# Kernel optimization log

Measured on AMD Instinct MI355X. Metric: run time of the kernel, lower is better.

The kernel has to match this reference:

```python
import jax, jax.numpy as jnp
import numpy as np

B, N, D, H = 2, 2048, 1024, 16
DH = D // H            # 64
PH = 3 * DH            # 192 per-head proj dim (module quirk: 3*Dh per head)
P = H * PH             # 3072 total projection width


def setup_inputs() -> dict:
    key = jax.random.key(0)
    ks = jax.random.split(key, 8)
    s = 0.02
    return {
        "input": jax.random.normal(ks[0], (B, N, D), dtype=jnp.float32),
        "q_w": jax.random.normal(ks[1], (D, P), dtype=jnp.float32) * s,
        "q_b": jnp.zeros((P,), dtype=jnp.float32),
        "k_w": jax.random.normal(ks[2], (D, P), dtype=jnp.float32) * s,
        "k_b": jnp.zeros((P,), dtype=jnp.float32),
        "v_w": jax.random.normal(ks[3], (D, P), dtype=jnp.float32) * s,
        "v_b": jnp.zeros((P,), dtype=jnp.float32),
        "o_w": jax.random.normal(ks[4], (P, D), dtype=jnp.float32) * s,
        "o_b": jnp.zeros((D,), dtype=jnp.float32),
    }


def reference(input, q_w, q_b, k_w, k_b, v_w, v_b, o_w, o_b):
    def heads(y):  # [B,N,H*PH] -> [B,H,N,PH]
        return y.reshape(B, N, H, PH).transpose(0, 2, 1, 3)

    q_mat = heads(input @ q_w + q_b)
    # faithful to source: v_mat uses the 'k' projection, k_mat uses the 'v' projection
    v_mat = heads(input @ k_w + k_b)
    k_mat = heads(input @ v_w + v_b)

    scale = 1.0 / jnp.sqrt(jnp.float32(DH * H))  # sqrt(dim), per source
    scores = jnp.einsum('bhnd,bhmd->bhnm', q_mat, k_mat) * scale
    weights = jax.nn.softmax(scores, axis=-1)
    inter = jnp.einsum('bhnm,bhmd->bhnd', weights, v_mat)
    inter = inter.transpose(0, 2, 1, 3).reshape(B, N, P)  # b n (h d)
    return inter @ o_w + o_b
```

## Files before the change

kernel.cpp:

```cpp
#include <hip/hip_runtime.h>
#include <cstdint>
#include <cstddef>

typedef __bf16 bf16;
typedef __attribute__((ext_vector_type(8))) __bf16 bf16x8;
typedef __attribute__((ext_vector_type(4))) __bf16 bf16x4;
typedef __attribute__((ext_vector_type(2))) __bf16 bf16x2;
typedef __attribute__((ext_vector_type(4))) float f32x4;

#define MFMA_16x16x32(a, b, c) __builtin_amdgcn_mfma_f32_16x16x32_bf16((a), (b), (c), 0, 0, 0)

__device__ __forceinline__ void gload_lds16(const void* g, void* l) {
  __builtin_amdgcn_global_load_lds((__attribute__((address_space(1))) void*)g,
                                   (__attribute__((address_space(3))) void*)l,
                                   16, 0, 0);
}

__global__ __launch_bounds__(256) void cvt_x_kernel(const float* __restrict__ in,
                                                    bf16* __restrict__ out) {
  int i = blockIdx.x * 256 + threadIdx.x;
  float4 v = ((const float4*)in)[i];
  bf16x4 o = {(bf16)v.x, (bf16)v.y, (bf16)v.z, (bf16)v.w};
  ((bf16x4*)out)[i] = o;
}

__global__ __launch_bounds__(256) void transpose_cvt_kernel(const float* __restrict__ in,
                                                            bf16* __restrict__ out,
                                                            int R, int C) {
  __shared__ float tile[32][33];
  int tiles_c = C >> 5;
  int br = (int)blockIdx.x / tiles_c, bc = (int)blockIdx.x % tiles_c;
  int r0 = br << 5, c0 = bc << 5;
  int tr = threadIdx.x >> 5, tc = threadIdx.x & 31;
#pragma unroll
  for (int i = 0; i < 4; i++)
    tile[tr + 8 * i][tc] = in[(size_t)(r0 + tr + 8 * i) * C + c0 + tc];
  __syncthreads();
#pragma unroll
  for (int i = 0; i < 4; i++) {
    int oc = tr + 8 * i;
    out[(size_t)(c0 + oc) * R + r0 + tc] = (bf16)tile[tc][oc];
  }
}

__global__ __launch_bounds__(256) void transpose_cvt3_kernel(const float* __restrict__ q_w,
                                                             const float* __restrict__ v_w,
                                                             const float* __restrict__ k_w,
                                                             bf16* __restrict__ out) {
  __shared__ float tile[32][33];
  int widx = (int)blockIdx.x / 3072;
  int blk = (int)blockIdx.x % 3072;
  const float* in = widx == 0 ? q_w : (widx == 1 ? v_w : k_w);
  bf16* o = out + (size_t)widx * 3072 * 1024;
  int br = blk / 96, bc = blk % 96;
  int r0 = br << 5, c0 = bc << 5;
  int tr = threadIdx.x >> 5, tc = threadIdx.x & 31;
#pragma unroll
  for (int i = 0; i < 4; i++)
    tile[tr + 8 * i][tc] = in[(size_t)(r0 + tr + 8 * i) * 3072 + c0 + tc];
  __syncthreads();
#pragma unroll
  for (int i = 0; i < 4; i++) {
    int oc = tr + 8 * i;
    o[(size_t)(c0 + oc) * 1024 + r0 + tc] = (bf16)tile[tc][oc];
  }
}

__global__ __launch_bounds__(512, 2) void gemm_fused_qkv(
    const bf16* __restrict__ A, const bf16* __restrict__ Bt,
    const float* __restrict__ q_b, const float* __restrict__ v_b,
    const float* __restrict__ k_b,
    bf16* __restrict__ Qm, bf16* __restrict__ Km, bf16* __restrict__ Vt) {
  constexpr int K = 1024, NT = 16;
  __shared__ __align__(16) bf16 sA[2][2][128 * 32];
  __shared__ __align__(16) bf16 sB[2][192 * 64];

  int bid = blockIdx.x;
  int xcd = bid & 7, j = bid >> 3;
  int bm = xcd * 4 + (j & 3), bn = j >> 2;
  int m0 = bm << 7, n0 = bn * 192;

  int tid = threadIdx.x, lane = tid & 63, w = tid >> 6;
  int wr = w >> 2, wc = w & 3;
  int l15 = lane & 15, lg = lane >> 4;

  int sra = lane >> 2, sca = lane & 3;
  const bf16* gA = A + (size_t)(m0 + w * 16 + sra) * K + ((sca ^ ((sra >> 1) & 3)) * 8);
  int srb = lane >> 3, scb = lane & 7;
  const bf16* gB = Bt + (size_t)(n0 + w * 24 + srb) * K + ((scb ^ srb) * 8);

#define STAGE_AB(BUF, T)                                                   \
  {                                                                        \
    _Pragma("unroll") for (int kh = 0; kh < 2; kh++)                       \
        gload_lds16(gA + (size_t)(T) * 64 + kh * 32, &sA[BUF][kh][w * 512]); \
    _Pragma("unroll") for (int ii = 0; ii < 3; ii++)                       \
        gload_lds16(gB + (size_t)(ii * 8) * K + (T) * 64,                  \
                    &sB[BUF][(w * 3 + ii) * 512]);                         \
  }
#define VMCNT(N) asm volatile("s_waitcnt vmcnt(" #N ")" ::: "memory")
#define LGK0                                           \
  {                                                    \
    asm volatile("s_waitcnt lgkmcnt(0)" ::: "memory"); \
    __builtin_amdgcn_sched_barrier(0);                 \
  }

  int slotA = lg ^ ((l15 >> 1) & 3);
  int aBase = wr * 2048 + l15 * 32 + slotA * 8;
  int bBase = (wc * 48 + l15) * 64;
  int sB0 = (lg ^ (l15 & 7)) * 8;
  int sB1 = ((4 + lg) ^ (l15 & 7)) * 8;

#define RD_A(BUF, KH)                                                      \
  _Pragma("unroll") for (int mf = 0; mf < 4; mf++)                         \
      a[mf] = *(const bf16x8*)&sA[BUF][KH][aBase + mf * 512];
#define RD_B(BUF, SLOT)                                                    \
  _Pragma("unroll") for (int nf = 0; nf < 3; nf++)                         \
      b[nf] = *(const bf16x8*)&sB[BUF][bBase + nf * 1024 + (SLOT)];
#define MFMA12                                                             \
  _Pragma("unroll") for (int mf = 0; mf < 4; mf++)                         \
      _Pragma("unroll") for (int nf = 0; nf < 3; nf++)                     \
          acc[mf][nf] = MFMA_16x16x32(a[mf], b[nf], acc[mf][nf]);

  f32x4 acc[4][3];
#pragma unroll
  for (int mf = 0; mf < 4; mf++)
#pragma unroll
    for (int nf = 0; nf < 3; nf++) acc[mf][nf] = (f32x4){0.f, 0.f, 0.f, 0.f};

  STAGE_AB(0, 0);

#pragma unroll 2
  for (int s = 0; s < NT; s++) {
    int buf = s & 1, nbuf = buf ^ 1;
    int nxt = (s + 1) & (NT - 1);
    bf16x8 a[4], b[3];

    STAGE_AB(nbuf, nxt);
    VMCNT(5);
    __builtin_amdgcn_s_barrier();

    RD_A(buf, 0);
    RD_B(buf, sB0);
    LGK0;
    __builtin_amdgcn_s_setprio(1);
    MFMA12;
    __builtin_amdgcn_s_setprio(0);

    RD_A(buf, 1);
    RD_B(buf, sB1);
    LGK0;
    __builtin_amdgcn_s_barrier();
    __builtin_amdgcn_s_setprio(1);
    MFMA12;
    __builtin_amdgcn_s_setprio(0);
  }

  int seg = bn >> 4;
  int segbn = bn & 15;
  const float* bias = seg == 0 ? q_b : (seg == 1 ? v_b : k_b);
  bf16* outQK = seg == 0 ? Qm : Km;
#pragma unroll
  for (int mf = 0; mf < 4; mf++) {
#pragma unroll
    for (int nf = 0; nf < 3; nf++) {
      int colL = segbn * 192 + wc * 48 + nf * 16 + l15;
      int row0 = m0 + wr * 64 + mf * 16 + lg * 4;
      float bv = bias[colL];
      if (seg < 2) {
#pragma unroll
        for (int r = 0; r < 4; r++)
          outQK[(size_t)(row0 + r) * 3072 + colL] = (bf16)(acc[mf][nf][r] + bv);
      } else {
        int hh = colL / 192, dd = colL % 192;
        int bi = row0 >> 11, nn = row0 & 2047;
        bf16x4 pk = {(bf16)(acc[mf][nf][0] + bv), (bf16)(acc[mf][nf][1] + bv),
                     (bf16)(acc[mf][nf][2] + bv), (bf16)(acc[mf][nf][3] + bv)};
        *(bf16x4*)(Vt + (((size_t)bi * 16 + hh) * 192 + dd) * 2048 + nn) = pk;
      }
    }
  }
#undef STAGE_AB
#undef RD_A
#undef RD_B
#undef MFMA12
}

__global__ __launch_bounds__(256, 3) void gemm_oproj(const bf16* __restrict__ A,
                                                     const bf16* __restrict__ Bt,
                                                     const float* __restrict__ bias,
                                                     float* __restrict__ out) {
  constexpr int K = 3072, NT = 48;
  __shared__ __align__(16) bf16 sA[2][2][128 * 32];
  __shared__ __align__(16) bf16 sB[2][2][64 * 32];

  int bid = blockIdx.x;
  int xcd = bid & 7, j = bid >> 3;
  int bm = xcd * 4 + (j & 3), bn = j >> 2;
  int m0 = bm << 7, n0 = bn << 6;

  int tid = threadIdx.x, lane = tid & 63, w = tid >> 6;
  int wr = w >> 1, wc = w & 1;
  int l15 = lane & 15, lg = lane >> 4;

  int sra = lane >> 2, sca = lane & 3;
  int swzS = (sca ^ ((sra >> 1) & 3)) * 8;
  const bf16* gA = A + (size_t)(m0 + w * 32 + sra) * K + swzS;
  const bf16* gB = Bt + (size_t)(n0 + w * 16 + sra) * K + swzS;

#define O_STAGE(BUF, T)                                                     \
  {                                                                         \
    _Pragma("unroll") for (int kh = 0; kh < 2; kh++) {                      \
      _Pragma("unroll") for (int ii = 0; ii < 2; ii++)                      \
          gload_lds16(gA + (size_t)(ii * 16) * K + (T) * 64 + kh * 32,      \
                      &sA[BUF][kh][(w * 32 + ii * 16) * 32]);               \
      gload_lds16(gB + (size_t)(T) * 64 + kh * 32, &sB[BUF][kh][w * 512]);  \
    }                                                                       \
  }

  int slotA = lg ^ ((l15 >> 1) & 3);
  int aBase = (wr * 64 + l15) * 32 + slotA * 8;
  int bBase = (wc * 32 + l15) * 32 + slotA * 8;

#define O_RD(BUF, KH)                                                      \
  {                                                                        \
    _Pragma("unroll") for (int mf = 0; mf < 4; mf++)                       \
        a[mf] = *(const bf16x8*)&sA[BUF][KH][aBase + mf * 512];             \
    _Pragma("unroll") for (int nf = 0; nf < 2; nf++)                       \
        b[nf] = *(const bf16x8*)&sB[BUF][KH][bBase + nf * 512];             \
  }
#define O_MFMA8                                                            \
  _Pragma("unroll") for (int mf = 0; mf < 4; mf++)                         \
      _Pragma("unroll") for (int nf = 0; nf < 2; nf++)                     \
          acc[mf][nf] = MFMA_16x16x32(a[mf], b[nf], acc[mf][nf]);

  f32x4 acc[4][2];
#pragma unroll
  for (int mf = 0; mf < 4; mf++)
#pragma unroll
    for (int nf = 0; nf < 2; nf++) acc[mf][nf] = (f32x4){0.f, 0.f, 0.f, 0.f};

  O_STAGE(0, 0);

#pragma unroll 2
  for (int s = 0; s < NT; s++) {
    int buf = s & 1, nbuf = buf ^ 1;
    int nxt = s + 1 < NT ? s + 1 : 0;
    bf16x8 a[4], b[2];

    O_STAGE(nbuf, nxt);
    VMCNT(6);
    __builtin_amdgcn_s_barrier();

    O_RD(buf, 0);
    LGK0;
    __builtin_amdgcn_s_setprio(1);
    O_MFMA8;
    __builtin_amdgcn_s_setprio(0);

    O_RD(buf, 1);
    LGK0;
    __builtin_amdgcn_s_barrier();
    __builtin_amdgcn_s_setprio(1);
    O_MFMA8;
    __builtin_amdgcn_s_setprio(0);
  }

#pragma unroll
  for (int mf = 0; mf < 4; mf++) {
#pragma unroll
    for (int nf = 0; nf < 2; nf++) {
      int col = n0 + wc * 32 + nf * 16 + l15;
      int row0 = m0 + wr * 64 + mf * 16 + lg * 4;
      float bv = bias[col];
#pragma unroll
      for (int r = 0; r < 4; r++)
        out[(size_t)(row0 + r) * 1024 + col] = acc[mf][nf][r] + bv;
    }
  }
#undef O_STAGE
#undef O_RD
#undef O_MFMA8
#undef VMCNT
#undef LGK0
}

__global__ __launch_bounds__(512, 2) void attn_kernel(const bf16* __restrict__ Q,
                                                      const bf16* __restrict__ Km,
                                                      const bf16* __restrict__ Vt,
                                                      bf16* __restrict__ inter) {
  __shared__ __align__(16) bf16 sK[2][64 * 192];
  __shared__ __align__(16) bf16 sV[2][192 * 64];
  __shared__ __align__(16) bf16 sPT[8 * 2 * 16 * 72];

  int i = blockIdx.x;
  int j = i >> 3;
  int bh = (i & 7) * 4 + (j >> 3);
  int qt = j & 7;
  int b = bh >> 4, h = bh & 15;
  int tid = threadIdx.x, lane = tid & 63, w = tid >> 6;
  int l15 = lane & 15, lg = lane >> 4;
  int swz = l15 & 7;

  const bf16* Qh = Q + (size_t)b * 2048 * 3072 + (size_t)h * 192;
  const bf16* Kh = Km + (size_t)b * 2048 * 3072 + (size_t)h * 192;
  const bf16* Vh = Vt + (size_t)bh * 192 * 2048;

  int q0 = qt * 256 + w * 32;

  int kOff[3], vOff[3], ldsOff[3];
#pragma unroll
  for (int ii = 0; ii < 3; ii++) {
    int r = ii * 8 + w;
    int s = r * 64 + lane;
    int krow = s / 24, kc = s % 24;
    int kcs = (kc & 24) | ((kc & 7) ^ (krow & 7));
    kOff[ii] = krow * 3072 + kcs * 8;
    int vrow = s >> 3, vc = s & 7;
    int vcs = vc ^ (vrow & 7);
    vOff[ii] = vrow * 2048 + vcs * 8;
    ldsOff[ii] = r * 512;
  }

#define STAGE(BUF, KT)                                                      \
  {                                                                         \
    int kb = (KT) * 64;                                                     \
    _Pragma("unroll") for (int ii = 0; ii < 3; ii++) {                      \
      gload_lds16(Kh + (size_t)kb * 3072 + kOff[ii], &sK[BUF][ldsOff[ii]]); \
      gload_lds16(Vh + kb + vOff[ii], &sV[BUF][ldsOff[ii]]);                \
    }                                                                       \
  }

  STAGE(0, 0);

  bf16x8 aq[2][6];
#pragma unroll
  for (int rf = 0; rf < 2; rf++)
#pragma unroll
    for (int kc = 0; kc < 6; kc++)
      aq[rf][kc] = *(const bf16x8*)(Qh + (size_t)(q0 + rf * 16 + l15) * 3072 + kc * 32 + lg * 8);

  f32x4 o[2][12];
#pragma unroll
  for (int rf = 0; rf < 2; rf++)
#pragma unroll
    for (int df = 0; df < 12; df++) o[rf][df] = (f32x4){0.f, 0.f, 0.f, 0.f};
  float mrow[2] = {-1e30f, -1e30f};
  float lrow[2] = {0.f, 0.f};

  const float scl2 = 0.03125f * 1.44269504f;

  bf16* myPT0 = &sPT[((w * 2 + 0) * 16 + l15) * 72];
  bf16* myPT1 = &sPT[((w * 2 + 1) * 16 + l15) * 72];

  __syncthreads();

  for (int kt = 0; kt < 32; kt++) {
    const bf16* kbuf = sK[kt & 1];
    const bf16* vbuf = sV[kt & 1];
    if (kt < 31) STAGE((kt & 1) ^ 1, kt + 1);

    f32x4 st[4][2];
#pragma unroll
    for (int kf = 0; kf < 4; kf++)
#pragma unroll
      for (int rf = 0; rf < 2; rf++) st[kf][rf] = (f32x4){0.f, 0.f, 0.f, 0.f};
    __builtin_amdgcn_s_setprio(1);
#pragma unroll
    for (int kc = 0; kc < 6; kc++) {
      int g = kc * 4 + lg;
      int cc = (g & 24) | ((g & 7) ^ swz);
#pragma unroll
      for (int kf = 0; kf < 4; kf++) {
        bf16x8 bk = *(const bf16x8*)&kbuf[(kf * 16 + l15) * 192 + cc * 8];
        st[kf][0] = MFMA_16x16x32(bk, aq[0][kc], st[kf][0]);
        st[kf][1] = MFMA_16x16x32(bk, aq[1][kc], st[kf][1]);
      }
    }
    __builtin_amdgcn_s_setprio(0);

#pragma unroll
    for (int rf = 0; rf < 2; rf++) {
      bf16* myPT = rf ? myPT1 : myPT0;
      float mk[4];
#pragma unroll
      for (int kf = 0; kf < 4; kf++)
        mk[kf] = fmaxf(fmaxf(st[kf][rf][0], st[kf][rf][1]),
                       fmaxf(st[kf][rf][2], st[kf][rf][3]));
      float pmx = fmaxf(fmaxf(mk[0], mk[1]), fmaxf(mk[2], mk[3]));
      pmx = fmaxf(pmx, __shfl_xor(pmx, 16));
      pmx = fmaxf(pmx, __shfl_xor(pmx, 32));
      float pms = pmx * scl2;

      float mn = mrow[rf];
      if (!__all(pms - mn <= 11.0f)) {
        mn = fmaxf(mn, pms);
        float corr = exp2f(mrow[rf] - mn);
        mrow[rf] = mn;
        lrow[rf] *= corr;
#pragma unroll
        for (int df = 0; df < 12; df++) o[rf][df] *= corr;
      }

      float skf[4];
#pragma unroll
      for (int kf = 0; kf < 4; kf++) {
        float e0 = exp2f(fmaf(st[kf][rf][0], scl2, -mn));
        float e1 = exp2f(fmaf(st[kf][rf][1], scl2, -mn));
        float e2 = exp2f(fmaf(st[kf][rf][2], scl2, -mn));
        float e3 = exp2f(fmaf(st[kf][rf][3], scl2, -mn));
        skf[kf] = (e0 + e1) + (e2 + e3);
        bf16x4 pk4 = {(bf16)e0, (bf16)e1, (bf16)e2, (bf16)e3};
        *(bf16x4*)&myPT[kf * 16 + 4 * lg] = pk4;
      }
      float rs = (skf[0] + skf[1]) + (skf[2] + skf[3]);
      rs += __shfl_xor(rs, 16);
      rs += __shfl_xor(rs, 32);
      lrow[rf] += rs;
    }

    bf16x8 pf[2][2];
#pragma unroll
    for (int rf = 0; rf < 2; rf++) {
      bf16* myPT = rf ? myPT1 : myPT0;
#pragma unroll
      for (int ks = 0; ks < 2; ks++)
        pf[rf][ks] = *(const bf16x8*)&myPT[ks * 32 + lg * 8];
    }

    __builtin_amdgcn_s_setprio(1);
#pragma unroll
    for (int ks = 0; ks < 2; ks++) {
      int cv = (ks * 4 + lg) ^ swz;
#pragma unroll
      for (int df = 0; df < 12; df++) {
        bf16x8 av = *(const bf16x8*)&vbuf[(df * 16 + l15) * 64 + cv * 8];
        o[0][df] = MFMA_16x16x32(av, pf[0][ks], o[0][df]);
        o[1][df] = MFMA_16x16x32(av, pf[1][ks], o[1][df]);
      }
    }
    __builtin_amdgcn_s_setprio(0);

    __syncthreads();
  }

#pragma unroll
  for (int rf = 0; rf < 2; rf++) {
    float inv = 1.0f / lrow[rf];
    size_t token = (size_t)b * 2048 + q0 + rf * 16 + l15;
    bf16* outp = inter + token * 3072 + h * 192 + lg * 4;
#pragma unroll
    for (int df = 0; df < 12; df++) {
      bf16x4 pk = {(bf16)(o[rf][df][0] * inv), (bf16)(o[rf][df][1] * inv),
                   (bf16)(o[rf][df][2] * inv), (bf16)(o[rf][df][3] * inv)};
      *(bf16x4*)(outp + df * 16) = pk;
    }
  }
#undef STAGE
}

extern "C" void kernel_launch(void* const* d_in, const int* in_sizes, int n_in,
                              void* d_out, int out_size, void* d_ws, size_t ws_size,
                              hipStream_t stream) {
  const float* X = (const float*)d_in[0];
  const float* q_w = (const float*)d_in[1];
  const float* q_b = (const float*)d_in[2];
  const float* k_w = (const float*)d_in[3];
  const float* k_b = (const float*)d_in[4];
  const float* v_w = (const float*)d_in[5];
  const float* v_b = (const float*)d_in[6];
  const float* o_w = (const float*)d_in[7];
  const float* o_b = (const float*)d_in[8];

  char* ws = (char*)d_ws;
  bf16* Xb  = (bf16*)(ws);
  bf16* Wqt = (bf16*)(ws + 8388608);
  bf16* Wot = (bf16*)(ws + 27262976);
  bf16* Qm  = (bf16*)(ws + 33554432);
  bf16* Km  = (bf16*)(ws + 58720256);
  bf16* Vtw = (bf16*)(ws + 83886080);
  bf16* Im  = (bf16*)(ws + 109051904);

  cvt_x_kernel<<<4096, 256, 0, stream>>>(X, Xb);
  transpose_cvt3_kernel<<<9216, 256, 0, stream>>>(q_w, v_w, k_w, Wqt);
  transpose_cvt_kernel<<<3072, 256, 0, stream>>>(o_w, Wot, 3072, 1024);

  gemm_fused_qkv<<<1536, 512, 0, stream>>>(Xb, Wqt, q_b, v_b, k_b, Qm, Km, Vtw);

  attn_kernel<<<256, 512, 0, stream>>>(Qm, Km, Vtw, Im);

  gemm_oproj<<<512, 256, 0, stream>>>(Im, Wot, o_b, (float*)d_out);
}
```

Before: 277.5 us.

## Merge prep conversions into one kernel and retile QKV GEMM to 64x128

Combines the input conversion and the two weight transpose-convert kernels into a single launch using block-index ranges. Retiles the fused QKV GEMM from 128x192 tiles with 512 threads to 64x128 tiles with 256 threads at 3 blocks per CU, with a new LDS layout and staging pattern. The aim is to cut launch overhead and improve occupancy and wave balance. The cost is lower per-block data reuse, which means more global and LDS traffic per FLOP.

```diff
diff --git a/kernel.cpp b/kernel.cpp
--- a/kernel.cpp
+++ b/kernel.cpp
@@ -10,26 +10,56 @@
 
 #define MFMA_16x16x32(a, b, c) __builtin_amdgcn_mfma_f32_16x16x32_bf16((a), (b), (c), 0, 0, 0)
 
+#define VMCNT(N) asm volatile("s_waitcnt vmcnt(" #N ")" ::: "memory")
+#define LGK0                                           \
+  {                                                    \
+    asm volatile("s_waitcnt lgkmcnt(0)" ::: "memory"); \
+    __builtin_amdgcn_sched_barrier(0);                 \
+  }
+
 __device__ __forceinline__ void gload_lds16(const void* g, void* l) {
   __builtin_amdgcn_global_load_lds((__attribute__((address_space(1))) void*)g,
                                    (__attribute__((address_space(3))) void*)l,
                                    16, 0, 0);
 }
 
-__global__ __launch_bounds__(256) void cvt_x_kernel(const float* __restrict__ in,
-                                                    bf16* __restrict__ out) {
-  int i = blockIdx.x * 256 + threadIdx.x;
-  float4 v = ((const float4*)in)[i];
-  bf16x4 o = {(bf16)v.x, (bf16)v.y, (bf16)v.z, (bf16)v.w};
-  ((bf16x4*)out)[i] = o;
-}
-
-__global__ __launch_bounds__(256) void transpose_cvt_kernel(const float* __restrict__ in,
-                                                            bf16* __restrict__ out,
-                                                            int R, int C) {
+__global__ __launch_bounds__(256) void prep_kernel(const float* __restrict__ X,
+                                                   const float* __restrict__ q_w,
+                                                   const float* __restrict__ v_w,
+                                                   const float* __restrict__ k_w,
+                                                   const float* __restrict__ o_w,
+                                                   bf16* __restrict__ Xb,
+                                                   bf16* __restrict__ Wqkv,
+                                                   bf16* __restrict__ Wot) {
   __shared__ float tile[32][33];
+  int blk = blockIdx.x;
+  if (blk < 4096) {
+    int i = blk * 256 + threadIdx.x;
+    float4 v = ((const float4*)X)[i];
+    bf16x4 o = {(bf16)v.x, (bf16)v.y, (bf16)v.z, (bf16)v.w};
+    ((bf16x4*)Xb)[i] = o;
+    return;
+  }
+  const float* in;
+  bf16* out;
+  int R, C, t;
+  if (blk < 13312) {
+    t = blk - 4096;
+    int widx = t / 3072;
+    t -= widx * 3072;
+    in = widx == 0 ? q_w : (widx == 1 ? v_w : k_w);
+    out = Wqkv + (size_t)widx * 3072 * 1024;
+    R = 1024;
+    C = 3072;
+  } else {
+    t = blk - 13312;
+    in = o_w;
+    out = Wot;
+    R = 3072;
+    C = 1024;
+  }
   int tiles_c = C >> 5;
-  int br = (int)blockIdx.x / tiles_c, bc = (int)blockIdx.x % tiles_c;
+  int br = t / tiles_c, bc = t % tiles_c;
   int r0 = br << 5, c0 = bc << 5;
   int tr = threadIdx.x >> 5, tc = threadIdx.x & 31;
 #pragma unroll
@@ -43,128 +73,97 @@
   }
 }
 
-__global__ __launch_bounds__(256) void transpose_cvt3_kernel(const float* __restrict__ q_w,
-                                                             const float* __restrict__ v_w,
-                                                             const float* __restrict__ k_w,
-                                                             bf16* __restrict__ out) {
-  __shared__ float tile[32][33];
-  int widx = (int)blockIdx.x / 3072;
-  int blk = (int)blockIdx.x % 3072;
-  const float* in = widx == 0 ? q_w : (widx == 1 ? v_w : k_w);
-  bf16* o = out + (size_t)widx * 3072 * 1024;
-  int br = blk / 96, bc = blk % 96;
-  int r0 = br << 5, c0 = bc << 5;
-  int tr = threadIdx.x >> 5, tc = threadIdx.x & 31;
-#pragma unroll
-  for (int i = 0; i < 4; i++)
-    tile[tr + 8 * i][tc] = in[(size_t)(r0 + tr + 8 * i) * 3072 + c0 + tc];
-  __syncthreads();
-#pragma unroll
-  for (int i = 0; i < 4; i++) {
-    int oc = tr + 8 * i;
-    o[(size_t)(c0 + oc) * 1024 + r0 + tc] = (bf16)tile[tc][oc];
-  }
-}
-
-__global__ __launch_bounds__(512, 2) void gemm_fused_qkv(
+__global__ __launch_bounds__(256, 3) void gemm_fused_qkv(
     const bf16* __restrict__ A, const bf16* __restrict__ Bt,
     const float* __restrict__ q_b, const float* __restrict__ v_b,
     const float* __restrict__ k_b,
     bf16* __restrict__ Qm, bf16* __restrict__ Km, bf16* __restrict__ Vt) {
   constexpr int K = 1024, NT = 16;
-  __shared__ __align__(16) bf16 sA[2][2][128 * 32];
-  __shared__ __align__(16) bf16 sB[2][192 * 64];
+  __shared__ __align__(16) bf16 sA[2][2][64 * 32];
+  __shared__ __align__(16) bf16 sB[2][2][128 * 32];
 
   int bid = blockIdx.x;
   int xcd = bid & 7, j = bid >> 3;
-  int bm = xcd * 4 + (j & 3), bn = j >> 2;
-  int m0 = bm << 7, n0 = bn * 192;
+  int bm = xcd * 8 + (j & 7), bn = j >> 3;
+  int m0 = bm << 6, n0 = bn << 7;
 
   int tid = threadIdx.x, lane = tid & 63, w = tid >> 6;
-  int wr = w >> 2, wc = w & 3;
+  int wr = w >> 1, wc = w & 1;
   int l15 = lane & 15, lg = lane >> 4;
 
   int sra = lane >> 2, sca = lane & 3;
-  const bf16* gA = A + (size_t)(m0 + w * 16 + sra) * K + ((sca ^ ((sra >> 1) & 3)) * 8);
-  int srb = lane >> 3, scb = lane & 7;
-  const bf16* gB = Bt + (size_t)(n0 + w * 24 + srb) * K + ((scb ^ srb) * 8);
-
-#define STAGE_AB(BUF, T)                                                   \
+  int swzS = (sca ^ ((sra >> 1) & 3)) * 8;
+  const bf16* gA = A + (size_t)(m0 + w * 16 + sra) * K + swzS;
+  const bf16* gB = Bt + (size_t)(n0 + w * 32 + sra) * K + swzS;
+
+#define Q_STAGE(BUF, T)                                                     \
+  {                                                                         \
+    _Pragma("unroll") for (int kh = 0; kh < 2; kh++) {                      \
+      gload_lds16(gA + (size_t)(T) * 64 + kh * 32, &sA[BUF][kh][w * 512]);  \
+      _Pragma("unroll") for (int ii = 0; ii < 2; ii++)                      \
+          gload_lds16(gB + (size_t)(ii * 16) * K + (T) * 64 + kh * 32,      \
+                      &sB[BUF][kh][(w * 32 + ii * 16) * 32]);               \
+    }                                                                       \
+  }
+
+  int slotA = lg ^ ((l15 >> 1) & 3);
+  int aBase = (wr * 32 + l15) * 32 + slotA * 8;
+  int bBase = (wc * 64 + l15) * 32 + slotA * 8;
+
+#define Q_RD(BUF, KH)                                                      \
   {                                                                        \
-    _Pragma("unroll") for (int kh = 0; kh < 2; kh++)                       \
-        gload_lds16(gA + (size_t)(T) * 64 + kh * 32, &sA[BUF][kh][w * 512]); \
-    _Pragma("unroll") for (int ii = 0; ii < 3; ii++)                       \
-        gload_lds16(gB + (size_t)(ii * 8) * K + (T) * 64,                  \
-                    &sB[BUF][(w * 3 + ii) * 512]);                         \
-  }
-#define VMCNT(N) asm volatile("s_waitcnt vmcnt(" #N ")" ::: "memory")
-#define LGK0                                           \
-  {                                                    \
-    asm volatile("s_waitcnt lgkmcnt(0)" ::: "memory"); \
-    __builtin_amdgcn_sched_barrier(0);                 \
-  }
-
-  int slotA = lg ^ ((l15 >> 1) & 3);
-  int aBase = wr * 2048 + l15 * 32 + slotA * 8;
-  int bBase = (wc * 48 + l15) * 64;
-  int sB0 = (lg ^ (l15 & 7)) * 8;
-  int sB1 = ((4 + lg) ^ (l15 & 7)) * 8;
-
-#define RD_A(BUF, KH)                                                      \
-  _Pragma("unroll") for (int mf = 0; mf < 4; mf++)                         \
-      a[mf] = *(const bf16x8*)&sA[BUF][KH][aBase + mf * 512];
-#define RD_B(BUF, SLOT)                                                    \
-  _Pragma("unroll") for (int nf = 0; nf < 3; nf++)                         \
-      b[nf] = *(const bf16x8*)&sB[BUF][bBase + nf * 1024 + (SLOT)];
-#define MFMA12                                                             \
-  _Pragma("unroll") for (int mf = 0; mf < 4; mf++)                         \
-      _Pragma("unroll") for (int nf = 0; nf < 3; nf++)                     \
+    _Pragma("unroll") for (int mf = 0; mf < 2; mf++)                       \
+        a[mf] = *(const bf16x8*)&sA[BUF][KH][aBase + mf * 512];             \
+    _Pragma("unroll") for (int nf = 0; nf < 4; nf++)                       \
+        b[nf] = *(const bf16x8*)&sB[BUF][KH][bBase + nf * 512];             \
+  }
+#define Q_MFMA8                                                            \
+  _Pragma("unroll") for (int mf = 0; mf < 2; mf++)                         \
+      _Pragma("unroll") for (int nf = 0; nf < 4; nf++)                     \
           acc[mf][nf] = MFMA_16x16x32(a[mf], b[nf], acc[mf][nf]);
 
-  f32x4 acc[4][3];
-#pragma unroll
-  for (int mf = 0; mf < 4; mf++)
-#pragma unroll
-    for (int nf = 0; nf < 3; nf++) acc[mf][nf] = (f32x4){0.f, 0.f, 0.f, 0.f};
-
-  STAGE_AB(0, 0);
+  f32x4 acc[2][4];
+#pragma unroll
+  for (int mf = 0; mf < 2; mf++)
+#pragma unroll
+    for (int nf = 0; nf < 4; nf++) acc[mf][nf] = (f32x4){0.f, 0.f, 0.f, 0.f};
+
+  Q_STAGE(0, 0);
 
 #pragma unroll 2
   for (int s = 0; s < NT; s++) {
     int buf = s & 1, nbuf = buf ^ 1;
     int nxt = (s + 1) & (NT - 1);
-    bf16x8 a[4], b[3];
-
-    STAGE_AB(nbuf, nxt);
-    VMCNT(5);
+    bf16x8 a[2], b[4];
+
+    Q_STAGE(nbuf, nxt);
+    VMCNT(6);
     __builtin_amdgcn_s_barrier();
 
-    RD_A(buf, 0);
-    RD_B(buf, sB0);
+    Q_RD(buf, 0);
     LGK0;
     __builtin_amdgcn_s_setprio(1);
-    MFMA12;
-    __builtin_amdgcn_s_setprio(0);
-
-    RD_A(buf, 1);
-    RD_B(buf, sB1);
+    Q_MFMA8;
+    __builtin_amdgcn_s_setprio(0);
+
+    Q_RD(buf, 1);
     LGK0;
     __builtin_amdgcn_s_barrier();
     __builtin_amdgcn_s_setprio(1);
-    MFMA12;
-    __builtin_amdgcn_s_setprio(0);
-  }
-
-  int seg = bn >> 4;
-  int segbn = bn & 15;
+    Q_MFMA8;
+    __builtin_amdgcn_s_setprio(0);
+  }
+
+  int seg = bn / 24;
+  int segbn = bn - seg * 24;
   const float* bias = seg == 0 ? q_b : (seg == 1 ? v_b : k_b);
   bf16* outQK = seg == 0 ? Qm : Km;
 #pragma unroll
-  for (int mf = 0; mf < 4; mf++) {
-#pragma unroll
-    for (int nf = 0; nf < 3; nf++) {
-      int colL = segbn * 192 + wc * 48 + nf * 16 + l15;
-      int row0 = m0 + wr * 64 + mf * 16 + lg * 4;
+  for (int mf = 0; mf < 2; mf++) {
+#pragma unroll
+    for (int nf = 0; nf < 4; nf++) {
+      int colL = segbn * 128 + wc * 64 + nf * 16 + l15;
+      int row0 = m0 + wr * 32 + mf * 16 + lg * 4;
       float bv = bias[colL];
       if (seg < 2) {
 #pragma unroll
@@ -179,10 +178,9 @@
       }
     }
   }
-#undef STAGE_AB
-#undef RD_A
-#undef RD_B
-#undef MFMA12
+#undef Q_STAGE
+#undef Q_RD
+#undef Q_MFMA8
 }
 
 __global__ __launch_bounds__(256, 3) void gemm_oproj(const bf16* __restrict__ A,
@@ -280,8 +278,6 @@
 #undef O_STAGE
 #undef O_RD
 #undef O_MFMA8
-#undef VMCNT
-#undef LGK0
 }
 
 __global__ __launch_bounds__(512, 2) void attn_kernel(const bf16* __restrict__ Q,
@@ -480,11 +476,9 @@
   bf16* Vtw = (bf16*)(ws + 83886080);
   bf16* Im  = (bf16*)(ws + 109051904);
 
-  cvt_x_kernel<<<4096, 256, 0, stream>>>(X, Xb);
-  transpose_cvt3_kernel<<<9216, 256, 0, stream>>>(q_w, v_w, k_w, Wqt);
-  transpose_cvt_kernel<<<3072, 256, 0, stream>>>(o_w, Wot, 3072, 1024);
-
-  gemm_fused_qkv<<<1536, 512, 0, stream>>>(Xb, Wqt, q_b, v_b, k_b, Qm, Km, Vtw);
+  prep_kernel<<<16384, 256, 0, stream>>>(X, q_w, v_w, k_w, o_w, Xb, Wqt, Wot);
+
+  gemm_fused_qkv<<<4608, 256, 0, stream>>>(Xb, Wqt, q_b, v_b, k_b, Qm, Km, Vtw);
 
   attn_kernel<<<256, 512, 0, stream>>>(Qm, Km, Vtw, Im);
 
```

Result: slower. 290.2 us (+4.6%).
